# Optimization experiments

Hardware: AMD Instinct MI355X
Metric: run time of the kernel (lower is better)

The kernel has to match this reference:

```python
import jax, jax.numpy as jnp
import numpy as np

B, S, D = 4, 2048, 2048
H, K = 16, 128          # num_heads, intermediate_dim
FINAL = H * K           # 2048
VDIM = 2048             # vector_dim
EPS_LN = 1e-6
EPS_NORM = 1e-30


def setup_inputs() -> dict:
    key = jax.random.key(0)
    ks = jax.random.split(key, 8)
    x = jax.random.normal(ks[0], (B, S, D), dtype=jnp.float32)
    vector = jax.random.normal(ks[1], (B, VDIM), dtype=jnp.float32)
    W_att = jax.random.normal(ks[2], (D, H), dtype=jnp.float32) / np.sqrt(D)
    temperature = jnp.ones((1, 1, H), dtype=jnp.float32)
    W_values = jax.random.normal(ks[3], (D, H, K), dtype=jnp.float32) / np.sqrt(D)
    W_op = jax.random.normal(ks[4], (FINAL, VDIM), dtype=jnp.float32) / np.sqrt(FINAL)
    ff1 = jax.random.normal(ks[5], (VDIM + D, D), dtype=jnp.float32) / np.sqrt(VDIM + D)
    ff1_b = jnp.zeros((1, 1, D), dtype=jnp.float32)
    ff2 = jax.random.normal(ks[6], (D, D), dtype=jnp.float32) / np.sqrt(D)
    ff2_b = jnp.zeros((1, 1, D), dtype=jnp.float32)
    gamma = jnp.ones((D,), dtype=jnp.float32)
    beta = jnp.zeros((D,), dtype=jnp.float32)
    return {"x": x, "vector": vector, "W_att": W_att, "temperature": temperature,
            "W_values": W_values, "W_op": W_op, "ff1": ff1, "ff1_b": ff1_b,
            "ff2": ff2, "ff2_b": ff2_b, "gamma": gamma, "beta": beta}


def reference(x, vector, W_att, temperature, W_values, W_op, ff1, ff1_b, ff2, ff2_b, gamma, beta):
    b, s, d = x.shape
    # attention gate per (query) position -- [B,S,H]
    logits = jnp.matmul(x, W_att)
    logits = logits - jnp.max(logits, axis=-2, keepdims=True)
    w = jnp.exp(logits * temperature)
    # exact collapse of repeat+tril+normalize: A[b,i,j,h] = w[b,i,h]*tril[i,j]
    # denom[b,i,h] = w[b,i,h]*(i+1) + 1e-30  ->  out = coef * causal cumsum of v
    counts = jnp.arange(1, s + 1, dtype=x.dtype)[None, :, None]  # [1,S,1]
    coef = w / (w * counts + EPS_NORM)                            # [B,S,H]
    v = jnp.einsum('bsi,ihk->bshk', x, W_values)                  # [B,S,H,K]
    cum_v = jnp.cumsum(v, axis=1)                                 # prefix-sum over keys
    pooled = (coef[..., None] * cum_v).reshape(b, s, -1)          # [B,S,H*K]
    op = jnp.matmul(pooled, W_op) + vector[:, None, :]            # [B,S,VDIM]
    concat = jnp.concatenate([x, op], axis=-1)                    # [B,S,VDIM+D]
    h = jax.nn.relu(jnp.matmul(concat, ff1) + ff1_b)
    h = jax.nn.relu(jnp.matmul(h, ff2) + ff2_b)
    res = h + x
    mean = jnp.mean(res, axis=-1, keepdims=True)
    cen = res - mean
    var = jnp.mean(cen * cen, axis=-1, keepdims=True)
    return cen / jnp.sqrt(var + EPS_LN) * gamma + beta
```

## Files before the change

### kernel.cpp

```cpp
#include <hip/hip_runtime.h>
#include <stdint.h>

#define B_DIM 4
#define S_DIM 2048
#define D_DIM 2048
#define H_DIM 16
#define M_ROWS (B_DIM * S_DIM)
#define CONCAT_LD 4096
#define NCHUNK 32
#define CHLEN (S_DIM / NCHUNK)

#define BM 128
#define BN 128
#define BK 64

typedef __attribute__((ext_vector_type(8))) __bf16 bf16x8;
typedef __attribute__((ext_vector_type(4))) float f32x4;

__device__ inline unsigned short f2bf(float f) {
  union { float f; unsigned u; } x; x.f = f;
  unsigned r = x.u + 0x7fffu + ((x.u >> 16) & 1u);
  return (unsigned short)(r >> 16);
}
__device__ inline float bf2f(unsigned short s) {
  union { unsigned u; float f; } x; x.u = ((unsigned)s) << 16;
  return x.f;
}

__global__ __launch_bounds__(256) void xconv_logits_kernel(
    const float* __restrict__ x, const float* __restrict__ Watt,
    unsigned short* __restrict__ concat, float* __restrict__ logits) {
  int row = blockIdx.x, t = threadIdx.x;
  const float* xr = x + (size_t)row * D_DIM;
  unsigned short* cr = concat + (size_t)row * CONCAT_LD;
  float p[H_DIM];
#pragma unroll
  for (int h = 0; h < H_DIM; ++h) p[h] = 0.f;
#pragma unroll
  for (int i = 0; i < 8; ++i) {
    int k = t + i * 256;
    float xv = xr[k];
    cr[k] = f2bf(xv);
    const float* wr = Watt + (size_t)k * H_DIM;
#pragma unroll
    for (int h = 0; h < H_DIM; ++h) p[h] += xv * wr[h];
  }
  __shared__ float red[4][H_DIM];
  int l = t & 63, w = t >> 6;
#pragma unroll
  for (int h = 0; h < H_DIM; ++h) {
    float v = p[h];
    for (int off = 32; off; off >>= 1) v += __shfl_down(v, off);
    if (l == 0) red[w][h] = v;
  }
  __syncthreads();
  if (t < H_DIM)
    logits[(size_t)row * H_DIM + t] = red[0][t] + red[1][t] + red[2][t] + red[3][t];
}

__global__ __launch_bounds__(256) void transpose_conv_kernel(
    const float* __restrict__ src, unsigned short* __restrict__ dst,
    int R, int C, int ldd) {
  __shared__ float tile[32][33];
  int c0 = blockIdx.x * 32, r0 = blockIdx.y * 32;
  int tx = threadIdx.x & 31, ty = threadIdx.x >> 5;
#pragma unroll
  for (int i = 0; i < 32; i += 8)
    tile[ty + i][tx] = src[(size_t)(r0 + ty + i) * C + c0 + tx];
  __syncthreads();
#pragma unroll
  for (int i = 0; i < 32; i += 8)
    dst[(size_t)(c0 + ty + i) * ldd + r0 + tx] = f2bf(tile[tx][ty + i]);
}

__global__ __launch_bounds__(256) void convert_kernel(
    const float* __restrict__ src, unsigned short* __restrict__ dst) {
  int idx = (blockIdx.x * 256 + threadIdx.x) * 4;
  const float4 v = *(const float4*)(src + idx);
  ushort4 o;
  o.x = f2bf(v.x); o.y = f2bf(v.y); o.z = f2bf(v.z); o.w = f2bf(v.w);
  *(ushort4*)(dst + idx) = o;
}

__global__ __launch_bounds__(256) void coef_kernel(
    const float* __restrict__ logits, const float* __restrict__ temp, float* __restrict__ coef) {
  int b = blockIdx.x >> 4, h = blockIdx.x & 15;
  int t = threadIdx.x;
  const float* lg = logits + (size_t)b * S_DIM * H_DIM + h;
  float mx = -1e30f;
  for (int s = t; s < S_DIM; s += 256) mx = fmaxf(mx, lg[(size_t)s * H_DIM]);
  for (int off = 32; off; off >>= 1) mx = fmaxf(mx, __shfl_down(mx, off));
  __shared__ float red[4];
  if ((t & 63) == 0) red[t >> 6] = mx;
  __syncthreads();
  mx = fmaxf(fmaxf(red[0], red[1]), fmaxf(red[2], red[3]));
  float T = temp[h];
  float* cf = coef + (size_t)b * S_DIM * H_DIM + h;
  for (int s = t; s < S_DIM; s += 256) {
    float w = expf((lg[(size_t)s * H_DIM] - mx) * T);
    cf[(size_t)s * H_DIM] = w / (w * (float)(s + 1) + 1e-30f);
  }
}

__global__ __launch_bounds__(256) void bias2_partial_kernel(
    const float* __restrict__ vector, const float* __restrict__ ff1,
    float* __restrict__ part) {
  int n = blockIdx.x * 256 + threadIdx.x;
  int seg = blockIdx.y, b = blockIdx.z;
  const float* vr = vector + (size_t)b * 2048 + seg * 128;
  const float* fr = ff1 + (size_t)(2048 + seg * 128) * 2048 + n;
  float acc = 0.f;
#pragma unroll 8
  for (int j = 0; j < 128; ++j) acc += vr[j] * fr[(size_t)j * 2048];
  part[((size_t)seg * 4 + b) * 2048 + n] = acc;
}

__global__ __launch_bounds__(256) void bias2_reduce_kernel(
    const float* __restrict__ part, const float* __restrict__ ff1_b,
    float* __restrict__ bias2) {
  int n = blockIdx.x * 256 + threadIdx.x;
  int b = blockIdx.y;
  float acc = ff1_b[n];
#pragma unroll
  for (int s = 0; s < 16; ++s) acc += part[((size_t)s * 4 + b) * 2048 + n];
  bias2[(size_t)b * 2048 + n] = acc;
}

template <int MODE>
__global__ __launch_bounds__(256) void gemm_bt_kernel(
    const unsigned short* __restrict__ A, int lda,
    const unsigned short* __restrict__ Bt, int ldb, int K,
    void* __restrict__ outp, int ldo,
    const float* __restrict__ bias, const float* __restrict__ resid) {
  __shared__ unsigned short As[BM * BK];
  __shared__ unsigned short Bs[BN * BK];
  const int t = threadIdx.x;
  const int w = t >> 6, l = t & 63;
  const int wm = w & 1, wn = w >> 1;
  const int q = l >> 4, ln = l & 15;

  const int L = blockIdx.y * 16 + blockIdx.x;
  const int xcd = L & 7;
  const int W = L >> 3;
  const int bx = W & 15;
  const int by = (W >> 4) * 8 + xcd;
  const int m0 = by * BM, n0 = bx * BN;

  f32x4 acc[4][4];
#pragma unroll
  for (int i = 0; i < 4; ++i)
#pragma unroll
    for (int j = 0; j < 4; ++j) acc[i][j] = {0.f, 0.f, 0.f, 0.f};

  for (int k0 = 0; k0 < K; k0 += BK) {
    __syncthreads();
#pragma unroll
    for (int r = 0; r < 4; ++r) {
      int s = r * 256 + t;
      int row = s >> 3;
      int ch = (s & 7) ^ (row & 7);
      const unsigned short* ga = A + (size_t)(m0 + row) * lda + k0 + ch * 8;
      __builtin_amdgcn_global_load_lds(
          (const __attribute__((address_space(1))) void*)ga,
          (__attribute__((address_space(3))) void*)(As + (r * 256 + w * 64) * 8), 16, 0, 0);
      const unsigned short* gb = Bt + (size_t)(n0 + row) * ldb + k0 + ch * 8;
      __builtin_amdgcn_global_load_lds(
          (const __attribute__((address_space(1))) void*)gb,
          (__attribute__((address_space(3))) void*)(Bs + (r * 256 + w * 64) * 8), 16, 0, 0);
    }
    __syncthreads();
#pragma unroll
    for (int h = 0; h < 2; ++h) {
      bf16x8 af[4], bfr[4];
#pragma unroll
      for (int mt = 0; mt < 4; ++mt) {
        int ar = wm * 64 + mt * 16 + ln;
        af[mt] = *(const bf16x8*)&As[ar * BK + (((h * 4 + q) ^ (ar & 7)) * 8)];
      }
#pragma unroll
      for (int nt = 0; nt < 4; ++nt) {
        int br = wn * 64 + nt * 16 + ln;
        bfr[nt] = *(const bf16x8*)&Bs[br * BK + (((h * 4 + q) ^ (br & 7)) * 8)];
      }
#pragma unroll
      for (int mt = 0; mt < 4; ++mt)
#pragma unroll
        for (int nt = 0; nt < 4; ++nt)
          acc[mt][nt] = __builtin_amdgcn_mfma_f32_16x16x32_bf16(af[mt], bfr[nt], acc[mt][nt], 0, 0, 0);
    }
  }

#pragma unroll
  for (int mt = 0; mt < 4; ++mt) {
#pragma unroll
    for (int i = 0; i < 4; ++i) {
      int row = m0 + wm * 64 + mt * 16 + q * 4 + i;
#pragma unroll
      for (int nt = 0; nt < 4; ++nt) {
        int col = n0 + wn * 64 + nt * 16 + ln;
        float vv = acc[mt][nt][i];
        if (MODE == 2) { vv += bias[(size_t)(row >> 11) * 2048 + col]; vv = fmaxf(vv, 0.f); }
        if (MODE == 4) {
          vv += bias[col]; vv = fmaxf(vv, 0.f);
          vv += resid[(size_t)row * 2048 + col];
          ((float*)outp)[(size_t)row * ldo + col] = vv;
        } else {
          ((unsigned short*)outp)[(size_t)row * ldo + col] = f2bf(vv);
        }
      }
    }
  }
}

#define GLD16(g, s)                                                        \
  __builtin_amdgcn_global_load_lds(                                        \
      (const __attribute__((address_space(1))) void*)(g),                  \
      (__attribute__((address_space(3))) void*)(s), 16, 0, 0)
#define BARX() asm volatile("s_barrier" ::: "memory")
#define VMW8() asm volatile("s_waitcnt vmcnt(8)" ::: "memory")
#define VMW0() asm volatile("s_waitcnt vmcnt(0)" ::: "memory")

template <int MODE>
__global__ __launch_bounds__(512, 2) void gemm256_kernel(
    const unsigned short* __restrict__ A, int lda,
    const unsigned short* __restrict__ Bt, int ldb, int K,
    void* __restrict__ outp, int ldo,
    const float* __restrict__ bias, const float* __restrict__ resid) {
  __shared__ unsigned short As[2][2][256 * 32];
  __shared__ unsigned short Bs[2][2][256 * 32];
  const int t = threadIdx.x;
  const int wv = t >> 6, l = t & 63;
  const int wm = wv >> 2, wn = wv & 3;
  const int q = l >> 4, ln = l & 15;

  const int L = blockIdx.y * 8 + blockIdx.x;
  const int lin = (L & 7) * 32 + (L >> 3);
  const int m0 = (lin >> 3) * 256, n0 = (lin & 7) * 256;

  const int srow = t >> 2;
  const int scol = (((t & 3) * 16) ^ (((srow >> 1) & 3) << 4)) >> 1;
  const unsigned short* Abase = A + (size_t)(m0 + srow) * lda + scol;
  const unsigned short* Bbase = Bt + (size_t)(n0 + srow) * ldb + scol;
  const size_t astep = (size_t)128 * lda, bstep = (size_t)128 * ldb;
  const int axor = ((ln >> 1) & 3) << 3;

  f32x4 acc[8][4];
#pragma unroll
  for (int i = 0; i < 8; ++i)
#pragma unroll
    for (int j = 0; j < 4; ++j) acc[i][j] = {0.f, 0.f, 0.f, 0.f};

  auto stageA = [&](int kt, int kh, int buf) {
    const unsigned short* g = Abase + (size_t)kt * 64 + kh * 32;
    GLD16(g, &As[buf][kh][wv * 512]);
    GLD16(g + astep, &As[buf][kh][4096 + wv * 512]);
  };
  auto stageB = [&](int kt, int kh, int buf) {
    const unsigned short* g = Bbase + (size_t)kt * 64 + kh * 32;
    GLD16(g, &Bs[buf][kh][wv * 512]);
    GLD16(g + bstep, &Bs[buf][kh][4096 + wv * 512]);
  };

  bf16x8 a[8], b[2];
  auto loadA = [&](int buf, int h) {
#pragma unroll
    for (int mt = 0; mt < 8; ++mt) {
      int ar = wm * 128 + mt * 16 + ln;
      a[mt] = *(const bf16x8*)&As[buf][h][ar * 32 + ((q * 8) ^ axor)];
    }
  };
  auto loadB2 = [&](int buf, int h, int np) {
#pragma unroll
    for (int i = 0; i < 2; ++i) {
      int br = wn * 64 + (np * 2 + i) * 16 + ln;
      b[i] = *(const bf16x8*)&Bs[buf][h][br * 32 + ((q * 8) ^ axor)];
    }
  };
  auto mm = [&](int np) {
    __builtin_amdgcn_s_setprio(1);
#pragma unroll
    for (int mt = 0; mt < 8; ++mt)
#pragma unroll
      for (int i = 0; i < 2; ++i)
        acc[mt][np * 2 + i] =
            __builtin_amdgcn_mfma_f32_16x16x32_bf16(a[mt], b[i], acc[mt][np * 2 + i], 0, 0, 0);
    __builtin_amdgcn_s_setprio(0);
  };

  const int NT = K >> 6;
  stageA(0, 0, 0); stageB(0, 0, 0);
  stageA(0, 1, 0); stageB(0, 1, 0);
  stageA(1, 0, 1); stageB(1, 0, 1);
  VMW8();
  BARX();

  for (int tt = 0; tt < NT; ++tt) {
    const int c = tt & 1;
    const int t1 = (tt + 1 == NT) ? 0 : tt + 1;
    const int t2 = (tt + 2 >= NT) ? tt + 2 - NT : tt + 2;
    loadA(c, 0); loadB2(c, 0, 0);
    stageA(t1, 1, c ^ 1);
    BARX();
    mm(0);
    BARX();
    loadB2(c, 0, 1);
    stageB(t1, 1, c ^ 1);
    BARX();
    mm(1);
    VMW8();
    BARX();
    loadA(c, 1); loadB2(c, 1, 0);
    stageA(t2, 0, c);
    BARX();
    mm(0);
    BARX();
    loadB2(c, 1, 1);
    stageB(t2, 0, c);
    BARX();
    mm(1);
    VMW8();
    BARX();
  }
  VMW0();

#pragma unroll
  for (int mt = 0; mt < 8; ++mt) {
#pragma unroll
    for (int i = 0; i < 4; ++i) {
      int row = m0 + wm * 128 + mt * 16 + q * 4 + i;
#pragma unroll
      for (int nt = 0; nt < 4; ++nt) {
        int col = n0 + wn * 64 + nt * 16 + ln;
        float vv = acc[mt][nt][i];
        if (MODE == 2) { vv += bias[(size_t)(row >> 11) * 2048 + col]; vv = fmaxf(vv, 0.f); }
        if (MODE == 4) {
          vv += bias[col]; vv = fmaxf(vv, 0.f);
          vv += resid[(size_t)row * 2048 + col];
          ((float*)outp)[(size_t)row * ldo + col] = vv;
        } else {
          ((unsigned short*)outp)[(size_t)row * ldo + col] = f2bf(vv);
        }
      }
    }
  }
}

__global__ __launch_bounds__(256) void scan_partial_kernel(
    const unsigned short* __restrict__ v, float* __restrict__ csum) {
  int c = blockIdx.x * 256 + threadIdx.x;
  int chunk = blockIdx.y, b = blockIdx.z;
  const unsigned short* p = v + ((size_t)(b * S_DIM + chunk * CHLEN)) * D_DIM + c;
  float s = 0.f;
#pragma unroll 4
  for (int i = 0; i < CHLEN; ++i) s += bf2f(p[(size_t)i * D_DIM]);
  csum[((size_t)b * NCHUNK + chunk) * D_DIM + c] = s;
}

__global__ __launch_bounds__(256) void scan_offsets_kernel(float* __restrict__ csum) {
  int c = blockIdx.x * 256 + threadIdx.x;
  int b = blockIdx.y;
  float run = 0.f;
  float* p = csum + (size_t)b * NCHUNK * D_DIM + c;
  for (int ch = 0; ch < NCHUNK; ++ch) {
    float tv = p[(size_t)ch * D_DIM];
    p[(size_t)ch * D_DIM] = run;
    run += tv;
  }
}

__global__ __launch_bounds__(256) void scan_apply_kernel(
    const unsigned short* __restrict__ v, const float* __restrict__ csum,
    const float* __restrict__ coef, unsigned short* __restrict__ pooled_out) {
  int c = blockIdx.x * 256 + threadIdx.x;
  int chunk = blockIdx.y, b = blockIdx.z;
  int h = c >> 7;
  int row0 = b * S_DIM + chunk * CHLEN;
  float run = csum[((size_t)b * NCHUNK + chunk) * D_DIM + c];
  const unsigned short* vp = v + (size_t)row0 * D_DIM + c;
  unsigned short* po = pooled_out + (size_t)row0 * CONCAT_LD + c;
  const float* cf = coef + (size_t)row0 * H_DIM + h;
#pragma unroll 4
  for (int i = 0; i < CHLEN; ++i) {
    run += bf2f(vp[(size_t)i * D_DIM]);
    po[(size_t)i * CONCAT_LD] = f2bf(cf[(size_t)i * H_DIM] * run);
  }
}

__global__ __launch_bounds__(256) void ln_kernel(
    float* __restrict__ out, const float* __restrict__ gamma, const float* __restrict__ beta) {
  int row = blockIdx.x, t = threadIdx.x;
  float* pr = out + (size_t)row * D_DIM;
  float vals[8];
  float s = 0.f;
#pragma unroll
  for (int i = 0; i < 8; ++i) { vals[i] = pr[t + i * 256]; s += vals[i]; }
  __shared__ float red[4];
  for (int off = 32; off; off >>= 1) s += __shfl_down(s, off);
  if ((t & 63) == 0) red[t >> 6] = s;
  __syncthreads();
  float mean = (red[0] + red[1] + red[2] + red[3]) * (1.f / D_DIM);
  __syncthreads();
  float c2 = 0.f;
#pragma unroll
  for (int i = 0; i < 8; ++i) { float c = vals[i] - mean; c2 += c * c; }
  for (int off = 32; off; off >>= 1) c2 += __shfl_down(c2, off);
  if ((t & 63) == 0) red[t >> 6] = c2;
  __syncthreads();
  float var = (red[0] + red[1] + red[2] + red[3]) * (1.f / D_DIM);
  float rstd = rsqrtf(var + 1e-6f);
#pragma unroll
  for (int i = 0; i < 8; ++i) {
    int col = t + i * 256;
    pr[col] = (vals[i] - mean) * rstd * gamma[col] + beta[col];
  }
}

extern "C" void kernel_launch(void* const* d_in, const int* in_sizes, int n_in,
                              void* d_out, int out_size, void* d_ws, size_t ws_size,
                              hipStream_t stream) {
  const float* x      = (const float*)d_in[0];
  const float* vector = (const float*)d_in[1];
  const float* W_att  = (const float*)d_in[2];
  const float* temp   = (const float*)d_in[3];
  const float* W_val  = (const float*)d_in[4];
  const float* W_op   = (const float*)d_in[5];
  const float* ff1    = (const float*)d_in[6];
  const float* ff1_b  = (const float*)d_in[7];
  const float* ff2    = (const float*)d_in[8];
  const float* ff2_b  = (const float*)d_in[9];
  const float* gamma  = (const float*)d_in[10];
  const float* beta   = (const float*)d_in[11];
  float* out = (float*)d_out;

  char* ws = (char*)d_ws;
  auto alloc = [&](size_t bytes) {
    char* p = ws; ws += (bytes + 255) & ~(size_t)255; return p;
  };
  unsigned short* concat = (unsigned short*)alloc((size_t)M_ROWS * CONCAT_LD * 2);
  unsigned short* wv_t   = (unsigned short*)alloc((size_t)2048 * 2048 * 2);
  unsigned short* btff1  = (unsigned short*)alloc((size_t)2048 * 4096 * 2);
  unsigned short* f1bT   = (unsigned short*)alloc((size_t)2048 * 2048 * 2);
  unsigned short* wop_bf = (unsigned short*)alloc((size_t)2048 * 2048 * 2);
  unsigned short* ff2_t  = (unsigned short*)alloc((size_t)2048 * 2048 * 2);
  unsigned short* vbuf   = (unsigned short*)alloc((size_t)M_ROWS * 2048 * 2);
  unsigned short* h1     = (unsigned short*)alloc((size_t)M_ROWS * 2048 * 2);
  float* logits = (float*)alloc((size_t)M_ROWS * H_DIM * 4);
  float* coef   = (float*)alloc((size_t)M_ROWS * H_DIM * 4);
  float* csum   = (float*)alloc((size_t)B_DIM * NCHUNK * D_DIM * 4);
  float* part   = (float*)alloc((size_t)16 * 4 * 2048 * 4);
  float* bias2  = (float*)alloc((size_t)4 * 2048 * 4);

  xconv_logits_kernel<<<M_ROWS, 256, 0, stream>>>(x, W_att, concat, logits);
  transpose_conv_kernel<<<dim3(64, 64), 256, 0, stream>>>(W_val, wv_t, 2048, 2048, 2048);
  transpose_conv_kernel<<<dim3(64, 64), 256, 0, stream>>>(ff1, btff1, 2048, 2048, 4096);
  transpose_conv_kernel<<<dim3(64, 64), 256, 0, stream>>>(ff1 + (size_t)2048 * 2048, f1bT, 2048, 2048, 2048);
  convert_kernel<<<2048 * 2048 / 1024, 256, 0, stream>>>(W_op, wop_bf);
  transpose_conv_kernel<<<dim3(64, 64), 256, 0, stream>>>(ff2, ff2_t, 2048, 2048, 2048);
  coef_kernel<<<B_DIM * H_DIM, 256, 0, stream>>>(logits, temp, coef);
  gemm_bt_kernel<1><<<dim3(16, 16), 256, 0, stream>>>(
      f1bT, 2048, wop_bf, 2048, 2048, btff1 + 2048, 4096, nullptr, nullptr);
  bias2_partial_kernel<<<dim3(8, 16, 4), 256, 0, stream>>>(vector, ff1, part);
  bias2_reduce_kernel<<<dim3(8, 4), 256, 0, stream>>>(part, ff1_b, bias2);
  gemm256_kernel<1><<<dim3(8, 32), 512, 0, stream>>>(
      concat, CONCAT_LD, wv_t, 2048, 2048, vbuf, 2048, nullptr, nullptr);
  scan_partial_kernel<<<dim3(8, NCHUNK, B_DIM), 256, 0, stream>>>(vbuf, csum);
  scan_offsets_kernel<<<dim3(8, B_DIM), 256, 0, stream>>>(csum);
  scan_apply_kernel<<<dim3(8, NCHUNK, B_DIM), 256, 0, stream>>>(vbuf, csum, coef, concat + 2048);
  gemm256_kernel<2><<<dim3(8, 32), 512, 0, stream>>>(
      concat, CONCAT_LD, btff1, 4096, 4096, h1, 2048, bias2, nullptr);
  gemm256_kernel<4><<<dim3(8, 32), 512, 0, stream>>>(
      h1, 2048, ff2_t, 2048, 2048, out, 2048, ff2_b, x);
  ln_kernel<<<M_ROWS, 256, 0, stream>>>(out, gamma, beta);
}
```

Baseline: 664.7 us.

## Merge weight prep kernels, fold scan offsets into apply, tweak GEMM prologue wait

Merges the four transpose-convert launches and the W_op convert into one 3D-grid prep kernel. Drops the scan_offsets kernel, so each scan_apply thread sums the preceding chunk totals itself. The GEMM prologue now waits at vmcnt(4) instead of vmcnt(8), and the LDS swizzle offset is precomputed once. The aim is fewer launches and less serial scan work, at the cost of redundant chunk-sum reads and a stricter initial load wait.

Measured after the change: 651.4 us. 2.0% less time.

```diff
diff --git a/kernel.cpp b/kernel.cpp
--- a/kernel.cpp
+++ b/kernel.cpp
@@ -58,28 +58,38 @@
     logits[(size_t)row * H_DIM + t] = red[0][t] + red[1][t] + red[2][t] + red[3][t];
 }
 
-__global__ __launch_bounds__(256) void transpose_conv_kernel(
-    const float* __restrict__ src, unsigned short* __restrict__ dst,
-    int R, int C, int ldd) {
+__global__ __launch_bounds__(256) void prep_kernel(
+    const float* __restrict__ Wval, const float* __restrict__ ff1,
+    const float* __restrict__ ff2, const float* __restrict__ Wop,
+    unsigned short* __restrict__ wv_t, unsigned short* __restrict__ btff1,
+    unsigned short* __restrict__ f1bT, unsigned short* __restrict__ ff2_t,
+    unsigned short* __restrict__ wop_bf) {
+  int z = blockIdx.z;
+  if (z == 4) {
+    size_t idx = (((size_t)blockIdx.y * 64 + blockIdx.x) * 256 + threadIdx.x) * 4;
+    const float4 v = *(const float4*)(Wop + idx);
+    ushort4 o;
+    o.x = f2bf(v.x); o.y = f2bf(v.y); o.z = f2bf(v.z); o.w = f2bf(v.w);
+    *(ushort4*)(wop_bf + idx) = o;
+    return;
+  }
+  const float* src;
+  unsigned short* dst;
+  int ldd;
+  if (z == 0)      { src = Wval;                        dst = wv_t;  ldd = 2048; }
+  else if (z == 1) { src = ff1;                         dst = btff1; ldd = 4096; }
+  else if (z == 2) { src = ff1 + (size_t)2048 * 2048;   dst = f1bT;  ldd = 2048; }
+  else             { src = ff2;                         dst = ff2_t; ldd = 2048; }
   __shared__ float tile[32][33];
   int c0 = blockIdx.x * 32, r0 = blockIdx.y * 32;
   int tx = threadIdx.x & 31, ty = threadIdx.x >> 5;
 #pragma unroll
   for (int i = 0; i < 32; i += 8)
-    tile[ty + i][tx] = src[(size_t)(r0 + ty + i) * C + c0 + tx];
+    tile[ty + i][tx] = src[(size_t)(r0 + ty + i) * 2048 + c0 + tx];
   __syncthreads();
 #pragma unroll
   for (int i = 0; i < 32; i += 8)
     dst[(size_t)(c0 + ty + i) * ldd + r0 + tx] = f2bf(tile[tx][ty + i]);
-}
-
-__global__ __launch_bounds__(256) void convert_kernel(
-    const float* __restrict__ src, unsigned short* __restrict__ dst) {
-  int idx = (blockIdx.x * 256 + threadIdx.x) * 4;
-  const float4 v = *(const float4*)(src + idx);
-  ushort4 o;
-  o.x = f2bf(v.x); o.y = f2bf(v.y); o.z = f2bf(v.z); o.w = f2bf(v.w);
-  *(ushort4*)(dst + idx) = o;
 }
 
 __global__ __launch_bounds__(256) void coef_kernel(
@@ -218,6 +228,7 @@
       (__attribute__((address_space(3))) void*)(s), 16, 0, 0)
 #define BARX() asm volatile("s_barrier" ::: "memory")
 #define VMW8() asm volatile("s_waitcnt vmcnt(8)" ::: "memory")
+#define VMW4() asm volatile("s_waitcnt vmcnt(4)" ::: "memory")
 #define VMW0() asm volatile("s_waitcnt vmcnt(0)" ::: "memory")
 
 template <int MODE>
@@ -242,7 +253,7 @@
   const unsigned short* Abase = A + (size_t)(m0 + srow) * lda + scol;
   const unsigned short* Bbase = Bt + (size_t)(n0 + srow) * ldb + scol;
   const size_t astep = (size_t)128 * lda, bstep = (size_t)128 * ldb;
-  const int axor = ((ln >> 1) & 3) << 3;
+  const int rsel = (q * 8) ^ (((ln >> 1) & 3) << 3);
 
   f32x4 acc[8][4];
 #pragma unroll
@@ -266,14 +277,14 @@
 #pragma unroll
     for (int mt = 0; mt < 8; ++mt) {
       int ar = wm * 128 + mt * 16 + ln;
-      a[mt] = *(const bf16x8*)&As[buf][h][ar * 32 + ((q * 8) ^ axor)];
+      a[mt] = *(const bf16x8*)&As[buf][h][ar * 32 + rsel];
     }
   };
   auto loadB2 = [&](int buf, int h, int np) {
 #pragma unroll
     for (int i = 0; i < 2; ++i) {
       int br = wn * 64 + (np * 2 + i) * 16 + ln;
-      b[i] = *(const bf16x8*)&Bs[buf][h][br * 32 + ((q * 8) ^ axor)];
+      b[i] = *(const bf16x8*)&Bs[buf][h][br * 32 + rsel];
     }
   };
   auto mm = [&](int np) {
@@ -291,7 +302,7 @@
   stageA(0, 0, 0); stageB(0, 0, 0);
   stageA(0, 1, 0); stageB(0, 1, 0);
   stageA(1, 0, 1); stageB(1, 0, 1);
-  VMW8();
+  VMW4();
   BARX();
 
   for (int tt = 0; tt < NT; ++tt) {
@@ -356,18 +367,6 @@
   csum[((size_t)b * NCHUNK + chunk) * D_DIM + c] = s;
 }
 
-__global__ __launch_bounds__(256) void scan_offsets_kernel(float* __restrict__ csum) {
-  int c = blockIdx.x * 256 + threadIdx.x;
-  int b = blockIdx.y;
-  float run = 0.f;
-  float* p = csum + (size_t)b * NCHUNK * D_DIM + c;
-  for (int ch = 0; ch < NCHUNK; ++ch) {
-    float tv = p[(size_t)ch * D_DIM];
-    p[(size_t)ch * D_DIM] = run;
-    run += tv;
-  }
-}
-
 __global__ __launch_bounds__(256) void scan_apply_kernel(
     const unsigned short* __restrict__ v, const float* __restrict__ csum,
     const float* __restrict__ coef, unsigned short* __restrict__ pooled_out) {
@@ -375,7 +374,9 @@
   int chunk = blockIdx.y, b = blockIdx.z;
   int h = c >> 7;
   int row0 = b * S_DIM + chunk * CHLEN;
-  float run = csum[((size_t)b * NCHUNK + chunk) * D_DIM + c];
+  const float* cs = csum + (size_t)b * NCHUNK * D_DIM + c;
+  float run = 0.f;
+  for (int j = 0; j < chunk; ++j) run += cs[(size_t)j * D_DIM];
   const unsigned short* vp = v + (size_t)row0 * D_DIM + c;
   unsigned short* po = pooled_out + (size_t)row0 * CONCAT_LD + c;
   const float* cf = coef + (size_t)row0 * H_DIM + h;
@@ -450,12 +451,9 @@
   float* part   = (float*)alloc((size_t)16 * 4 * 2048 * 4);
   float* bias2  = (float*)alloc((size_t)4 * 2048 * 4);
 
+  prep_kernel<<<dim3(64, 64, 5), 256, 0, stream>>>(
+      W_val, ff1, ff2, W_op, wv_t, btff1, f1bT, ff2_t, wop_bf);
   xconv_logits_kernel<<<M_ROWS, 256, 0, stream>>>(x, W_att, concat, logits);
-  transpose_conv_kernel<<<dim3(64, 64), 256, 0, stream>>>(W_val, wv_t, 2048, 2048, 2048);
-  transpose_conv_kernel<<<dim3(64, 64), 256, 0, stream>>>(ff1, btff1, 2048, 2048, 4096);
-  transpose_conv_kernel<<<dim3(64, 64), 256, 0, stream>>>(ff1 + (size_t)2048 * 2048, f1bT, 2048, 2048, 2048);
-  convert_kernel<<<2048 * 2048 / 1024, 256, 0, stream>>>(W_op, wop_bf);
-  transpose_conv_kernel<<<dim3(64, 64), 256, 0, stream>>>(ff2, ff2_t, 2048, 2048, 2048);
   coef_kernel<<<B_DIM * H_DIM, 256, 0, stream>>>(logits, temp, coef);
   gemm_bt_kernel<1><<<dim3(16, 16), 256, 0, stream>>>(
       f1bT, 2048, wop_bf, 2048, 2048, btff1 + 2048, 4096, nullptr, nullptr);
@@ -464,7 +462,6 @@
   gemm256_kernel<1><<<dim3(8, 32), 512, 0, stream>>>(
       concat, CONCAT_LD, wv_t, 2048, 2048, vbuf, 2048, nullptr, nullptr);
   scan_partial_kernel<<<dim3(8, NCHUNK, B_DIM), 256, 0, stream>>>(vbuf, csum);
-  scan_offsets_kernel<<<dim3(8, B_DIM), 256, 0, stream>>>(csum);
   scan_apply_kernel<<<dim3(8, NCHUNK, B_DIM), 256, 0, stream>>>(vbuf, csum, coef, concat + 2048);
   gemm256_kernel<2><<<dim3(8, 32), 512, 0, stream>>>(
       concat, CONCAT_LD, btff1, 4096, 4096, h1, 2048, bias2, nullptr);
```
